# Kernel optimization log

Measured on AMD Instinct MI355X. Metric: run time of the kernel, lower is better.

## Reference

```python
import jax, jax.numpy as jnp
import numpy as np

B, S, D, H = 32, 577, 768, 12
DH = D // H
MLP = 4 * D
EPS = 1e-5


def _layernorm(x, g, b):
    m = jnp.mean(x, axis=-1, keepdims=True)
    v = jnp.mean((x - m) ** 2, axis=-1, keepdims=True)
    return (x - m) * jax.lax.rsqrt(v + EPS) * g + b


def setup_inputs() -> dict:
    key = jax.random.key(0)
    ks = jax.random.split(key, 12)
    w = lambda k, shp: (jax.random.normal(k, shp, dtype=jnp.float32) * 0.02)
    return {
        "x": jax.random.normal(ks[0], (B, S, D), dtype=jnp.float32),
        "ln1_g": jnp.ones((D,), jnp.float32), "ln1_b": jnp.zeros((D,), jnp.float32),
        "ln2_g": jnp.ones((D,), jnp.float32), "ln2_b": jnp.zeros((D,), jnp.float32),
        "wq": w(ks[1], (H, DH, DH)), "bq": jnp.zeros((H, DH), jnp.float32),
        "wk": w(ks[2], (H, DH, DH)), "bk": jnp.zeros((H, DH), jnp.float32),
        "wv": w(ks[3], (H, DH, DH)), "bv": jnp.zeros((H, DH), jnp.float32),
        "w1": w(ks[4], (D, MLP)), "b1": jnp.zeros((MLP,), jnp.float32),
        "w2": w(ks[5], (MLP, D)), "b2": jnp.zeros((D,), jnp.float32),
    }


def reference(x, ln1_g, ln1_b, ln2_g, ln2_b, wq, bq, wk, bk, wv, bv, w1, b1, w2, b2):
    b, s, d = x.shape
    xn = _layernorm(x, ln1_g, ln1_b)
    xh = xn.reshape(b, s, H, DH)  # split heads along last dim (as in torch slicing)
    # per-head linear maps, batched over heads: [B,H,S,DH]
    q = jnp.einsum('bshd,hdo->bhso', xh, wq) + bq[:, None, :]
    k = jnp.einsum('bshd,hdo->bhso', xh, wk) + bk[:, None, :]
    v = jnp.einsum('bshd,hdo->bhso', xh, wv) + bv[:, None, :]
    scores = jnp.einsum('bhso,bhto->bhst', q, k) / (DH ** 0.5)
    attn = jax.nn.softmax(scores, axis=-1)  # softmax over keys (torch dim=1 of [S,S])
    o = jnp.einsum('bhst,bhtd->bshd', attn, v).reshape(b, s, d)
    out = x + o
    yn = _layernorm(out, ln2_g, ln2_b)
    h = jax.nn.gelu(yn @ w1 + b1, approximate=False)  # torch GELU default is erf-based
    return out + h @ w2 + b2
```

## Files before the change

### kernel.cpp

```cpp
#include <hip/hip_runtime.h>

#define S_LEN 577
#define SPAD  640
#define DMODEL 768
#define NH 12
#define DHEAD 64
#define MLPD 3072
#define NROWS (32 * 577)
#define MPAD  18688
#define NBH   (32 * 12)
#define LOG2E 1.44269504088896340736f

typedef __attribute__((ext_vector_type(8))) short s8v;
typedef __attribute__((ext_vector_type(4))) float f4v;

#define MFMA16(a, b, c) __builtin_amdgcn_mfma_f32_16x16x32_bf16((a), (b), (c), 0, 0, 0)

__device__ __forceinline__ short f2bf(float f) {
  union { float f; unsigned u; } a; a.f = f;
  unsigned r = a.u + 0x7FFFu + ((a.u >> 16) & 1u);
  return (short)(r >> 16);
}
__device__ __forceinline__ short f2bfF(float f) {
  union { float f; unsigned u; } a; a.f = f;
  return (short)((a.u + 0x8000u) >> 16);
}

__device__ __forceinline__ void gload16(const short* g, const short* l) {
  __builtin_amdgcn_global_load_lds(
      (const __attribute__((address_space(1))) void*)g,
      (__attribute__((address_space(3))) void*)l, 16, 0, 0);
}

__global__ __launch_bounds__(256) void transpose_w(const float* __restrict__ in,
                                                   short* __restrict__ out, int R, int C) {
  __shared__ float tile[32][33];
  int c0 = blockIdx.x * 32, r0 = blockIdx.y * 32;
  int tx = threadIdx.x, ty = threadIdx.y;
  for (int i = ty; i < 32; i += 8) tile[i][tx] = in[(size_t)(r0 + i) * C + c0 + tx];
  __syncthreads();
  for (int i = ty; i < 32; i += 8) out[(size_t)(c0 + i) * R + r0 + tx] = f2bf(tile[tx][i]);
}

__global__ __launch_bounds__(256) void prep_qkv(const float* __restrict__ wq, const float* __restrict__ wk,
                                                const float* __restrict__ wv, short* __restrict__ oq,
                                                short* __restrict__ ok, short* __restrict__ ov) {
  int h = blockIdx.x, t = threadIdx.x;
  const float* src0 = wq + (size_t)h * 4096;
  const float* src1 = wk + (size_t)h * 4096;
  const float* src2 = wv + (size_t)h * 4096;
  short* dst0 = oq + (size_t)h * 4096;
  short* dst1 = ok + (size_t)h * 4096;
  short* dst2 = ov + (size_t)h * 4096;
  for (int i = t; i < 4096; i += 256) {
    int o = i >> 6, d = i & 63;
    dst0[i] = f2bf(src0[d * 64 + o]);
    dst1[i] = f2bf(src1[d * 64 + o]);
    dst2[i] = f2bf(src2[d * 64 + o]);
  }
}

__global__ __launch_bounds__(256) void pad_kv(short* __restrict__ kg, short* __restrict__ vt) {
  int idx = blockIdx.x * 256 + threadIdx.x;
  const int padw = SPAD - S_LEN;
  const int per = DHEAD * padw;
  if (idx >= NBH * per) return;
  int bh = idx / per, r = idx - bh * per;
  int col = r / padw, s = S_LEN + (r - col * padw);
  vt[((size_t)bh * DHEAD + col) * SPAD + s] = 0;
  kg[((size_t)bh * SPAD + s) * DHEAD + col] = 0;
}

__global__ __launch_bounds__(256) void ln_kernel(const float* __restrict__ x, const float* __restrict__ g,
                                                 const float* __restrict__ bta, short* __restrict__ out) {
  int row = blockIdx.x;
  int t = threadIdx.x;
  const float* xr = x + (size_t)row * DMODEL;
  float v0 = xr[t], v1 = xr[t + 256], v2 = xr[t + 512];
  float s = v0 + v1 + v2;
  float s2 = v0 * v0 + v1 * v1 + v2 * v2;
  for (int o = 32; o; o >>= 1) { s += __shfl_down(s, o); s2 += __shfl_down(s2, o); }
  __shared__ float red[8];
  if ((t & 63) == 0) { int w = t >> 6; red[w] = s; red[4 + w] = s2; }
  __syncthreads();
  s = red[0] + red[1] + red[2] + red[3];
  s2 = red[4] + red[5] + red[6] + red[7];
  float m = s * (1.f / DMODEL);
  float rs = rsqrtf(s2 * (1.f / DMODEL) - m * m + 1e-5f);
  short* orow = out + (size_t)row * DMODEL;
  orow[t]       = f2bf((v0 - m) * rs * g[t]       + bta[t]);
  orow[t + 256] = f2bf((v1 - m) * rs * g[t + 256] + bta[t + 256]);
  orow[t + 512] = f2bf((v2 - m) * rs * g[t + 512] + bta[t + 512]);
}

__global__ __launch_bounds__(256) void qkv_kernel(const short* __restrict__ xn,
    const short* __restrict__ wqt, const short* __restrict__ wkt, const short* __restrict__ wvt,
    const float* __restrict__ bq, const float* __restrict__ bk, const float* __restrict__ bv,
    short* __restrict__ qg, short* __restrict__ kg, short* __restrict__ vt) {
  __shared__ __align__(16) short wl[3][64][72];
  int bid = blockIdx.x;
  int h = bid % NH, mt = bid / NH;
  int t = threadIdx.x;
  {
    int o = t >> 2, d0 = (t & 3) * 16;
    const short* s0 = wqt + (size_t)h * 4096 + o * 64 + d0;
    const short* s1 = wkt + (size_t)h * 4096 + o * 64 + d0;
    const short* s2 = wvt + (size_t)h * 4096 + o * 64 + d0;
    *(uint4*)&wl[0][o][d0]     = *(const uint4*)s0;
    *(uint4*)&wl[0][o][d0 + 8] = *(const uint4*)(s0 + 8);
    *(uint4*)&wl[1][o][d0]     = *(const uint4*)s1;
    *(uint4*)&wl[1][o][d0 + 8] = *(const uint4*)(s1 + 8);
    *(uint4*)&wl[2][o][d0]     = *(const uint4*)s2;
    *(uint4*)&wl[2][o][d0 + 8] = *(const uint4*)(s2 + 8);
  }
  __syncthreads();
  int w = t >> 6, l = t & 63, l15 = l & 15, lh = l >> 4;
  int m0 = mt * 64 + w * 16;
  if (m0 >= NROWS) return;
  f4v z = {0.f, 0.f, 0.f, 0.f};
  f4v aq[4], ak[4], av[4];
#pragma unroll
  for (int nt = 0; nt < 4; ++nt) { aq[nt] = z; ak[nt] = z; av[nt] = z; }
  const short* xrow = xn + (size_t)(m0 + l15) * DMODEL + h * DHEAD;
#pragma unroll
  for (int kk = 0; kk < 64; kk += 32) {
    s8v af = *(const s8v*)(xrow + kk + lh * 8);
#pragma unroll
    for (int nt = 0; nt < 4; ++nt) {
      s8v b0 = *(const s8v*)&wl[0][nt * 16 + l15][kk + lh * 8];
      s8v b1 = *(const s8v*)&wl[1][nt * 16 + l15][kk + lh * 8];
      s8v b2 = *(const s8v*)&wl[2][nt * 16 + l15][kk + lh * 8];
      aq[nt] = MFMA16(af, b0, aq[nt]);
      ak[nt] = MFMA16(af, b1, ak[nt]);
      av[nt] = MFMA16(af, b2, av[nt]);
    }
  }
#pragma unroll
  for (int nt = 0; nt < 4; ++nt) {
    int col = nt * 16 + l15;
    float biq = bq[h * DHEAD + col], bik = bk[h * DHEAD + col], biv = bv[h * DHEAD + col];
#pragma unroll
    for (int i = 0; i < 4; ++i) {
      int m = m0 + lh * 4 + i;
      int bb = m / S_LEN;
      int ss = m - bb * S_LEN;
      int bh = bb * NH + h;
      qg[((size_t)bh * S_LEN + ss) * DHEAD + col] = f2bf((aq[nt][i] + biq) * (0.125f * LOG2E));
      kg[((size_t)bh * SPAD + ss) * DHEAD + col]  = f2bf(ak[nt][i] + bik);
      vt[((size_t)bh * DHEAD + col) * SPAD + ss]  = f2bf(av[nt][i] + biv);
    }
  }
}

__global__ __launch_bounds__(256) void attn_kernel(const short* __restrict__ qg, const short* __restrict__ kg,
                                                   const short* __restrict__ vt, const float* __restrict__ x,
                                                   float* __restrict__ outp) {
  __shared__ __align__(16) short Pb[4][2][32][72];
  int bh = blockIdx.x;
  int qt = blockIdx.y;
  int h = bh % NH, b = bh / NH;
  int t = threadIdx.x, w = t >> 6, l = t & 63, l15 = l & 15, lh = l >> 4;
  int q0 = qt * 128 + w * 32;
  if (q0 > 576) return;
  size_t qbase = (size_t)bh * S_LEN * DHEAD;
  size_t kbase = (size_t)bh * SPAD * DHEAD;
  size_t vbase = (size_t)bh * DHEAD * SPAD;
  s8v aq[2][2];
#pragma unroll
  for (int f = 0; f < 2; ++f) {
    int qrow = q0 + f * 16 + l15; if (qrow > 576) qrow = 576;
    const short* qp = qg + qbase + (size_t)qrow * DHEAD + lh * 8;
    aq[f][0] = *(const s8v*)qp;
    aq[f][1] = *(const s8v*)(qp + 32);
  }
  f4v z = {0.f, 0.f, 0.f, 0.f};
  f4v z16 = {-16.f, -16.f, -16.f, -16.f};
  f4v acc[2][4];
  float lsum[2][4];
#pragma unroll
  for (int f = 0; f < 2; ++f) {
#pragma unroll
    for (int dt = 0; dt < 4; ++dt) acc[f][dt] = z;
#pragma unroll
    for (int i = 0; i < 4; ++i) lsum[f][i] = 0.f;
  }

#define LOADK(KB, K0, K1)                                              \
  {                                                                    \
    _Pragma("unroll")                                                  \
    for (int nt = 0; nt < 4; ++nt) {                                   \
      const short* kp = kg + kbase + (size_t)((KB) + nt * 16 + l15) * DHEAD + lh * 8; \
      K0[nt] = *(const s8v*)kp;                                        \
      K1[nt] = *(const s8v*)(kp + 32);                                 \
    }                                                                  \
  }

#define QKTILE(MASK)                                                   \
  {                                                                    \
    _Pragma("unroll")                                                  \
    for (int nt = 0; nt < 4; ++nt) {                                   \
      _Pragma("unroll")                                                \
      for (int f = 0; f < 2; ++f) {                                    \
        f4v a = MFMA16(aq[f][0], kf0[nt], z16);                        \
        a = MFMA16(aq[f][1], kf1[nt], a);                              \
        sc[f][nt] = a;                                                 \
      }                                                                \
    }                                                                  \
    if (MASK) {                                                        \
      _Pragma("unroll")                                                \
      for (int nt = 0; nt < 4; ++nt) {                                 \
        int col = 576 + nt * 16 + l15;                                 \
        if (col > 576) {                                               \
          _Pragma("unroll")                                            \
          for (int f = 0; f < 2; ++f) {                                \
            sc[f][nt][0] = sc[f][nt][1] = sc[f][nt][2] = sc[f][nt][3] = -1e30f; } \
        }                                                              \
      }                                                                \
    }                                                                  \
  }

#define SMAX(PAR)                                                      \
  {                                                                    \
    _Pragma("unroll")                                                  \
    for (int f = 0; f < 2; ++f)                                        \
      _Pragma("unroll")                                                \
      for (int i = 0; i < 4; ++i) {                                    \
        float s = lsum[f][i];                                          \
        _Pragma("unroll")                                              \
        for (int nt = 0; nt < 4; ++nt) {                               \
          float e = exp2f(sc[f][nt][i]);                               \
          s += e;                                                      \
          Pb[w][PAR][f * 16 + lh * 4 + i][nt * 16 + l15] = f2bfF(e);   \
        }                                                              \
        lsum[f][i] = s;                                                \
      }                                                                \
  }

  s8v kf0[4], kf1[4], kn0[4], kn1[4];
  f4v sc[2][4];
  LOADK(0, kf0, kf1);
  QKTILE(false);
  LOADK(64, kn0, kn1);
  SMAX(0);

  for (int kt = 0; kt < 10; ++kt) {
    int par = kt & 1;
    int kb = kt * 64;
    s8v vf[2][4];
#pragma unroll
    for (int kk2 = 0; kk2 < 2; ++kk2) {
      const short* vp = vt + vbase + kb + kk2 * 32 + lh * 8;
#pragma unroll
      for (int dt = 0; dt < 4; ++dt)
        vf[kk2][dt] = *(const s8v*)(vp + (size_t)(dt * 16 + l15) * SPAD);
    }
    if (kt < 9) {
#pragma unroll
      for (int nt = 0; nt < 4; ++nt) { kf0[nt] = kn0[nt]; kf1[nt] = kn1[nt]; }
      QKTILE(kt + 1 == 9);
      if (kt < 8) LOADK(kb + 128, kn0, kn1);
      SMAX(par ^ 1);
    }
#pragma unroll
    for (int kk2 = 0; kk2 < 2; ++kk2) {
      s8v af0 = *(const s8v*)&Pb[w][par][l15][kk2 * 32 + lh * 8];
      s8v af1 = *(const s8v*)&Pb[w][par][16 + l15][kk2 * 32 + lh * 8];
#pragma unroll
      for (int dt = 0; dt < 4; ++dt) {
        acc[0][dt] = MFMA16(af0, vf[kk2][dt], acc[0][dt]);
        acc[1][dt] = MFMA16(af1, vf[kk2][dt], acc[1][dt]);
      }
    }
  }
#undef LOADK
#undef QKTILE
#undef SMAX
#pragma unroll
  for (int f = 0; f < 2; ++f)
#pragma unroll
    for (int i = 0; i < 4; ++i) {
      float s = lsum[f][i];
      s += __shfl_xor(s, 1);
      s += __shfl_xor(s, 2);
      s += __shfl_xor(s, 4);
      s += __shfl_xor(s, 8);
      int srow = q0 + f * 16 + lh * 4 + i;
      if (srow > 576) continue;
      float inv = 1.f / s;
      size_t idx0 = ((size_t)b * S_LEN + srow) * DMODEL + h * DHEAD + l15;
#pragma unroll
      for (int dt = 0; dt < 4; ++dt) {
        size_t idx = idx0 + dt * 16;
        outp[idx] = x[idx] + acc[f][dt][i] * inv;
      }
    }
}

#define BARR asm volatile("s_barrier" ::: "memory")

#define STAGE_HALF(G, SH, bufi, half, ktile)                                       \
  do {                                                                             \
    _Pragma("unroll") for (int rd = 0; rd < 2; ++rd) {                             \
      int rw_ = rd * 64 + (tid >> 3);                                              \
      int sl_ = (tid & 7) ^ (rw_ & 7);                                             \
      gload16((G) + (size_t)((half) * 128 + rw_) * K + (ktile) * 64 + sl_ * 8,     \
              &SH[bufi][(half) * 128 + rw_][(tid & 7) * 8]);                       \
    }                                                                              \
  } while (0)

#define READ_A(rh)                                                                 \
  _Pragma("unroll") for (int mt = 0; mt < 4; ++mt)                                 \
    _Pragma("unroll") for (int kh = 0; kh < 2; ++kh)                               \
      af[mt][kh] = *(const s8v*)&sA[cur][(rh) * 128 + wr * 64 + mt * 16 + l15]     \
                                    [((kh * 4 + lh) ^ s7) * 8];

#define READ_B(BF, chh)                                                            \
  _Pragma("unroll") for (int nt = 0; nt < 2; ++nt)                                 \
    _Pragma("unroll") for (int kh = 0; kh < 2; ++kh)                               \
      BF[nt][kh] = *(const s8v*)&sB[cur][wc * 64 + (chh) * 32 + nt * 16 + l15]     \
                                    [((kh * 4 + lh) ^ s7) * 8];

#define DO_MFMA(rh, ch, BF)                                                        \
  __builtin_amdgcn_s_setprio(1);                                                   \
  _Pragma("unroll") for (int mt = 0; mt < 4; ++mt)                                 \
    _Pragma("unroll") for (int nt = 0; nt < 2; ++nt)                               \
      _Pragma("unroll") for (int kh = 0; kh < 2; ++kh)                             \
        acc[(rh) * 4 + mt][(ch) * 2 + nt] =                                        \
            MFMA16(af[mt][kh], BF[nt][kh], acc[(rh) * 4 + mt][(ch) * 2 + nt]);     \
  __builtin_amdgcn_s_setprio(0);

#define GEMM8_BODY                                                                 \
  int nwg = gridDim.x;                                                             \
  int orig = blockIdx.x;                                                           \
  int qq = nwg >> 3, rr = nwg & 7;                                                 \
  int xcd = orig & 7, lin = orig >> 3;                                             \
  int wg = (xcd < rr ? xcd * (qq + 1) : rr * (qq + 1) + (xcd - rr) * qq) + lin;    \
  int nx = N >> 8;                                                                 \
  int n0 = (wg % nx) * 256, m0 = (wg / nx) * 256;                                  \
  int tid = threadIdx.x;                                                           \
  int wid = tid >> 6, l = tid & 63, l15 = l & 15, lh = l >> 4;                     \
  int s7 = l15 & 7;                                                                \
  int wr = wid >> 2, wc = wid & 3;                                                 \
  const short* Ab = A + (size_t)m0 * K;                                            \
  const short* Bb = Bt + (size_t)n0 * K;                                           \
  f4v z = {0.f, 0.f, 0.f, 0.f};                                                    \
  f4v acc[8][4];                                                                   \
  _Pragma("unroll") for (int i = 0; i < 8; ++i)                                    \
    _Pragma("unroll") for (int j = 0; j < 4; ++j) acc[i][j] = z;                   \
  s8v af[4][2], bf0[2][2], bf1[2][2];                                              \
  int NT = K >> 6;                                                                 \
  STAGE_HALF(Ab, sA, 0, 0, 0); STAGE_HALF(Ab, sA, 0, 1, 0);                        \
  STAGE_HALF(Bb, sB, 0, 0, 0); STAGE_HALF(Bb, sB, 0, 1, 0);                        \
  STAGE_HALF(Ab, sA, 1, 0, 1); STAGE_HALF(Bb, sB, 1, 0, 1);                        \
  STAGE_HALF(Bb, sB, 1, 1, 1);                                                     \
  asm volatile("s_waitcnt vmcnt(6)" ::: "memory");                                 \
  BARR;                                                                            \
  int cur = 0;                                                                     \
  for (int kt = 0; kt < NT; ++kt) {                                                \
    int nxt = cur ^ 1;                                                             \
    READ_A(0); READ_B(bf0, 0);                                                     \
    if (kt + 1 < NT) STAGE_HALF(Ab, sA, nxt, 1, kt + 1);                           \
    BARR; DO_MFMA(0, 0, bf0); BARR;                                                \
    READ_B(bf1, 1);                                                                \
    if (kt + 2 < NT) STAGE_HALF(Ab, sA, cur, 0, kt + 2);                           \
    BARR; DO_MFMA(0, 1, bf1); BARR;                                                \
    READ_A(1);                                                                     \
    if (kt + 2 < NT) STAGE_HALF(Bb, sB, cur, 0, kt + 2);                           \
    BARR; DO_MFMA(1, 1, bf1); BARR;                                                \
    if (kt + 2 < NT) STAGE_HALF(Bb, sB, cur, 1, kt + 2);                           \
    BARR; DO_MFMA(1, 0, bf0);                                                      \
    if (kt < NT - 2)       { asm volatile("s_waitcnt vmcnt(6)" ::: "memory"); }    \
    else if (kt == NT - 2) { asm volatile("s_waitcnt vmcnt(0)" ::: "memory"); }    \
    BARR;                                                                          \
    cur = nxt;                                                                     \
  }

__global__ __launch_bounds__(512, 1) void gemm_gelu(const short* __restrict__ A, const short* __restrict__ Bt,
                                                    const float* __restrict__ bias, short* __restrict__ C,
                                                    int M, int N, int K) {
  __shared__ __align__(16) short sA[2][256][64];
  __shared__ __align__(16) short sB[2][256][64];
  GEMM8_BODY
#pragma unroll
  for (int ri = 0; ri < 8; ++ri)
#pragma unroll
    for (int ci = 0; ci < 4; ++ci) {
      int col = n0 + wc * 64 + (ci >> 1) * 32 + (ci & 1) * 16 + l15;
      float bi = bias[col];
#pragma unroll
      for (int i = 0; i < 4; ++i) {
        int row = m0 + (ri >> 2) * 128 + wr * 64 + (ri & 3) * 16 + lh * 4 + i;
        float v = acc[ri][ci][i] + bi;
        float u = v * (2.30221838f + 0.10294364f * v * v);
        v = v / (1.f + exp2f(-u));
        C[(size_t)row * N + col] = f2bf(v);
      }
    }
}

__global__ __launch_bounds__(512, 1) void gemm_res(const short* __restrict__ A, const short* __restrict__ Bt,
                                                   const float* __restrict__ bias, float* __restrict__ outp,
                                                   int Mvalid, int N, int K) {
  __shared__ __align__(16) short sA[2][256][64];
  __shared__ __align__(16) short sB[2][256][64];
  GEMM8_BODY
#pragma unroll
  for (int ri = 0; ri < 8; ++ri)
#pragma unroll
    for (int ci = 0; ci < 4; ++ci) {
      int col = n0 + wc * 64 + (ci >> 1) * 32 + (ci & 1) * 16 + l15;
      float bi = bias[col];
#pragma unroll
      for (int i = 0; i < 4; ++i) {
        int row = m0 + (ri >> 2) * 128 + wr * 64 + (ri & 3) * 16 + lh * 4 + i;
        if (row < Mvalid) {
          size_t idx = (size_t)row * N + col;
          outp[idx] += acc[ri][ci][i] + bi;
        }
      }
    }
}

extern "C" void kernel_launch(void* const* d_in, const int* in_sizes, int n_in,
                              void* d_out, int out_size, void* d_ws, size_t ws_size,
                              hipStream_t stream) {
  const float* x    = (const float*)d_in[0];
  const float* ln1g = (const float*)d_in[1];
  const float* ln1b = (const float*)d_in[2];
  const float* ln2g = (const float*)d_in[3];
  const float* ln2b = (const float*)d_in[4];
  const float* wq   = (const float*)d_in[5];
  const float* bq   = (const float*)d_in[6];
  const float* wk   = (const float*)d_in[7];
  const float* bk   = (const float*)d_in[8];
  const float* wv   = (const float*)d_in[9];
  const float* bv   = (const float*)d_in[10];
  const float* w1   = (const float*)d_in[11];
  const float* b1   = (const float*)d_in[12];
  const float* w2   = (const float*)d_in[13];
  const float* b2   = (const float*)d_in[14];
  float* outp = (float*)d_out;

  char* ws = (char*)d_ws;
  size_t off = 0;
  auto carve = [&](size_t elems) -> short* {
    short* p = (short*)(ws + off);
    off += elems * sizeof(short);
    off = (off + 255) & ~(size_t)255;
    return p;
  };
  short* yn   = carve((size_t)MPAD * DMODEL);
  short* w1t  = carve((size_t)MLPD * DMODEL);
  short* w2t  = carve((size_t)DMODEL * MLPD);
  short* wqt  = carve((size_t)NH * 64 * 64);
  short* wkt  = carve((size_t)NH * 64 * 64);
  short* wvt  = carve((size_t)NH * 64 * 64);
  size_t union_base = off;
  short* hbuf = carve((size_t)MPAD * MLPD);
  off = union_base;
  short* xn   = carve((size_t)NROWS * DMODEL);
  short* qg   = carve((size_t)NBH * S_LEN * DHEAD);
  short* kg   = carve((size_t)NBH * SPAD * DHEAD);
  short* vtb  = carve((size_t)NBH * DHEAD * SPAD);
  (void)ws_size; (void)in_sizes; (void)n_in; (void)out_size;

  transpose_w<<<dim3(MLPD / 32, DMODEL / 32), dim3(32, 8), 0, stream>>>(w1, w1t, DMODEL, MLPD);
  transpose_w<<<dim3(DMODEL / 32, MLPD / 32), dim3(32, 8), 0, stream>>>(w2, w2t, MLPD, DMODEL);
  prep_qkv<<<NH, 256, 0, stream>>>(wq, wk, wv, wqt, wkt, wvt);
  pad_kv<<<(NBH * DHEAD * (SPAD - S_LEN) + 255) / 256, 256, 0, stream>>>(kg, vtb);

  ln_kernel<<<NROWS, 256, 0, stream>>>(x, ln1g, ln1b, xn);

  qkv_kernel<<<((NROWS + 63) / 64) * NH, 256, 0, stream>>>(xn, wqt, wkt, wvt, bq, bk, bv, qg, kg, vtb);

  attn_kernel<<<dim3(NBH, 5), 256, 0, stream>>>(qg, kg, vtb, x, outp);

  ln_kernel<<<NROWS, 256, 0, stream>>>(outp, ln2g, ln2b, yn);

  gemm_gelu<<<dim3((MPAD / 256) * (MLPD / 256)), 512, 0, stream>>>(yn, w1t, b1, hbuf, MPAD, MLPD, DMODEL);
  gemm_res<<<dim3((MPAD / 256) * (DMODEL / 256)), 512, 0, stream>>>(hbuf, w2t, b2, outp, NROWS, DMODEL, MLPD);
}
```

Measured before the change: 533.4 us.

## Prefetch V tiles one step ahead and raise MFMA priority in attention loop

Restructures the attention inner loop so that V fragments for the next key tile are loaded a step in advance, alongside the K prefetch, instead of at the start of each iteration. MFMA sections are wrapped in s_setprio to favour matrix issue, the loop is fully unrolled, and launch bounds now request two blocks per SM. The aim is to hide global-load latency for V behind QK and softmax work. The cost is higher register pressure from the extra V buffers, which could spill under the tighter launch bound.

```diff
diff --git a/kernel.cpp b/kernel.cpp
--- a/kernel.cpp
+++ b/kernel.cpp
@@ -152,9 +152,9 @@
   }
 }
 
-__global__ __launch_bounds__(256) void attn_kernel(const short* __restrict__ qg, const short* __restrict__ kg,
-                                                   const short* __restrict__ vt, const float* __restrict__ x,
-                                                   float* __restrict__ outp) {
+__global__ __launch_bounds__(256, 2) void attn_kernel(const short* __restrict__ qg, const short* __restrict__ kg,
+                                                      const short* __restrict__ vt, const float* __restrict__ x,
+                                                      float* __restrict__ outp) {
   __shared__ __align__(16) short Pb[4][2][32][72];
   int bh = blockIdx.x;
   int qt = blockIdx.y;
@@ -185,18 +185,33 @@
     for (int i = 0; i < 4; ++i) lsum[f][i] = 0.f;
   }
 
-#define LOADK(KB, K0, K1)                                              \
+  s8v kf0[4], kf1[4], vf[2][4], vn[2][4];
+  f4v sc[2][4];
+
+#define LOADK(KB)                                                      \
   {                                                                    \
     _Pragma("unroll")                                                  \
     for (int nt = 0; nt < 4; ++nt) {                                   \
       const short* kp = kg + kbase + (size_t)((KB) + nt * 16 + l15) * DHEAD + lh * 8; \
-      K0[nt] = *(const s8v*)kp;                                        \
-      K1[nt] = *(const s8v*)(kp + 32);                                 \
+      kf0[nt] = *(const s8v*)kp;                                       \
+      kf1[nt] = *(const s8v*)(kp + 32);                                \
     }                                                                  \
   }
 
-#define QKTILE(MASK)                                                   \
+#define LOADV(KB, VF)                                                  \
   {                                                                    \
+    _Pragma("unroll")                                                  \
+    for (int kk2 = 0; kk2 < 2; ++kk2) {                                \
+      const short* vp = vt + vbase + (KB) + kk2 * 32 + lh * 8;         \
+      _Pragma("unroll")                                                \
+      for (int dt = 0; dt < 4; ++dt)                                   \
+        VF[kk2][dt] = *(const s8v*)(vp + (size_t)(dt * 16 + l15) * SPAD); \
+    }                                                                  \
+  }
+
+#define QKT()                                                          \
+  {                                                                    \
+    __builtin_amdgcn_s_setprio(1);                                     \
     _Pragma("unroll")                                                  \
     for (int nt = 0; nt < 4; ++nt) {                                   \
       _Pragma("unroll")                                                \
@@ -206,15 +221,18 @@
         sc[f][nt] = a;                                                 \
       }                                                                \
     }                                                                  \
-    if (MASK) {                                                        \
-      _Pragma("unroll")                                                \
-      for (int nt = 0; nt < 4; ++nt) {                                 \
-        int col = 576 + nt * 16 + l15;                                 \
-        if (col > 576) {                                               \
-          _Pragma("unroll")                                            \
-          for (int f = 0; f < 2; ++f) {                                \
-            sc[f][nt][0] = sc[f][nt][1] = sc[f][nt][2] = sc[f][nt][3] = -1e30f; } \
-        }                                                              \
+    __builtin_amdgcn_s_setprio(0);                                     \
+  }
+
+#define MASK9()                                                        \
+  {                                                                    \
+    _Pragma("unroll")                                                  \
+    for (int nt = 0; nt < 4; ++nt) {                                   \
+      int col = 576 + nt * 16 + l15;                                   \
+      if (col > 576) {                                                 \
+        _Pragma("unroll")                                              \
+        for (int f = 0; f < 2; ++f) {                                  \
+          sc[f][nt][0] = sc[f][nt][1] = sc[f][nt][2] = sc[f][nt][3] = -1e30f; } \
       }                                                                \
     }                                                                  \
   }
@@ -236,45 +254,52 @@
       }                                                                \
   }
 
-  s8v kf0[4], kf1[4], kn0[4], kn1[4];
-  f4v sc[2][4];
-  LOADK(0, kf0, kf1);
-  QKTILE(false);
-  LOADK(64, kn0, kn1);
+#define PVT(PAR)                                                       \
+  {                                                                    \
+    __builtin_amdgcn_s_setprio(1);                                     \
+    _Pragma("unroll")                                                  \
+    for (int kk2 = 0; kk2 < 2; ++kk2) {                                \
+      s8v af0 = *(const s8v*)&Pb[w][PAR][l15][kk2 * 32 + lh * 8];      \
+      s8v af1 = *(const s8v*)&Pb[w][PAR][16 + l15][kk2 * 32 + lh * 8]; \
+      _Pragma("unroll")                                                \
+      for (int dt = 0; dt < 4; ++dt) {                                 \
+        acc[0][dt] = MFMA16(af0, vf[kk2][dt], acc[0][dt]);             \
+        acc[1][dt] = MFMA16(af1, vf[kk2][dt], acc[1][dt]);             \
+      }                                                                \
+    }                                                                  \
+    __builtin_amdgcn_s_setprio(0);                                     \
+  }
+
+  LOADK(0);
+  LOADV(0, vf);
+  QKT();
+  LOADK(64);
   SMAX(0);
 
+#pragma unroll
   for (int kt = 0; kt < 10; ++kt) {
     int par = kt & 1;
-    int kb = kt * 64;
-    s8v vf[2][4];
-#pragma unroll
-    for (int kk2 = 0; kk2 < 2; ++kk2) {
-      const short* vp = vt + vbase + kb + kk2 * 32 + lh * 8;
-#pragma unroll
-      for (int dt = 0; dt < 4; ++dt)
-        vf[kk2][dt] = *(const s8v*)(vp + (size_t)(dt * 16 + l15) * SPAD);
-    }
     if (kt < 9) {
-#pragma unroll
-      for (int nt = 0; nt < 4; ++nt) { kf0[nt] = kn0[nt]; kf1[nt] = kn1[nt]; }
-      QKTILE(kt + 1 == 9);
-      if (kt < 8) LOADK(kb + 128, kn0, kn1);
+      QKT();
+      if (kt < 8) LOADK((kt + 2) * 64);
+      LOADV((kt + 1) * 64, vn);
+      if (kt == 8) MASK9();
       SMAX(par ^ 1);
     }
-#pragma unroll
-    for (int kk2 = 0; kk2 < 2; ++kk2) {
-      s8v af0 = *(const s8v*)&Pb[w][par][l15][kk2 * 32 + lh * 8];
-      s8v af1 = *(const s8v*)&Pb[w][par][16 + l15][kk2 * 32 + lh * 8];
-#pragma unroll
-      for (int dt = 0; dt < 4; ++dt) {
-        acc[0][dt] = MFMA16(af0, vf[kk2][dt], acc[0][dt]);
-        acc[1][dt] = MFMA16(af1, vf[kk2][dt], acc[1][dt]);
-      }
+    PVT(par);
+    if (kt < 9) {
+#pragma unroll
+      for (int kk2 = 0; kk2 < 2; ++kk2)
+#pragma unroll
+        for (int dt = 0; dt < 4; ++dt) vf[kk2][dt] = vn[kk2][dt];
     }
   }
 #undef LOADK
-#undef QKTILE
+#undef LOADV
+#undef QKT
+#undef MASK9
 #undef SMAX
+#undef PVT
 #pragma unroll
   for (int f = 0; f < 2; ++f)
 #pragma unroll
```

Result: slower. 761.7 us (+42.8%).
